# Performance work log

Hardware: AMD Instinct MI355X
Metric: run time of the kernel (lower is better)

The kernel has to match this reference:

```python
import jax, jax.numpy as jnp
import numpy as np

# Static config mirroring init_kwargs
N, C, H, W = 2, 10, 30, 30
PAD = 4                    # pad_size
HL = WL = 1 + 2 * PAD      # 9x9 local window
MAXH = MAXW = 10           # max_height / max_width
L = MAXH * MAXW            # tokens per pixel sequence = 100
D = C + 1                  # d_model = 11 (color channels + pad indicator)
EPS = 1e-5


def setup_inputs() -> dict:
    key = jax.random.key(0)
    ks = jax.random.split(key, 7)
    # one-hot ARC-style grid: each pixel is one of C colors
    classes = jax.random.randint(ks[0], (N, H, W), 0, C)
    x = jax.nn.one_hot(classes, C, dtype=jnp.float32).transpose(0, 3, 1, 2)  # [N,C,H,W]
    s = 0.1
    w_in = jax.random.normal(ks[1], (3 * D, D), dtype=jnp.float32) * s   # in_proj_weight
    w_out = jax.random.normal(ks[2], (D, D), dtype=jnp.float32) * s     # out_proj
    w_ff1 = jax.random.normal(ks[3], (1, D), dtype=jnp.float32) * s     # linear1 (D->1)
    w_ff2 = jax.random.normal(ks[4], (D, 1), dtype=jnp.float32) * s     # linear2 (1->D)
    ln1_g = jnp.ones((D,), dtype=jnp.float32)
    ln2_g = jnp.ones((D,), dtype=jnp.float32)
    return {"x": x, "w_in": w_in, "w_out": w_out, "w_ff1": w_ff1,
            "w_ff2": w_ff2, "ln1_g": ln1_g, "ln2_g": ln2_g}


def _layernorm(x, g):
    m = jnp.mean(x, axis=-1, keepdims=True)
    v = jnp.var(x, axis=-1, keepdims=True)
    return (x - m) / jnp.sqrt(v + EPS) * g


def reference(x, w_in, w_out, w_ff1, w_ff2, ln1_g, ln2_g):
    # pad colors with pad_value=0, pad-indicator channel with 1 in the border
    xp = jnp.pad(x, ((0, 0), (0, 0), (PAD, PAD), (PAD, PAD)))
    ind = jnp.pad(jnp.zeros((N, 1, H, W), x.dtype),
                  ((0, 0), (0, 0), (PAD, PAD), (PAD, PAD)), constant_values=1.0)
    xa = jnp.concatenate([xp, ind], axis=1).transpose(0, 2, 3, 1)  # [N,Hp,Wp,D]

    # im2col: 9x9 window around every pixel
    ii = jnp.arange(H)[:, None] + jnp.arange(HL)[None, :]  # [H,HL]
    jj = jnp.arange(W)[:, None] + jnp.arange(WL)[None, :]  # [W,WL]
    patches = xa[:, ii[:, None, :, None], jj[None, :, None, :], :]   # [N,H,W,HL,WL,D]
    patches = patches.transpose(0, 1, 2, 5, 3, 4)                    # [N,H,W,D,HL,WL]
    # embed window into max_height x max_width canvas (fill = pad_value = 0)
    patches = jnp.pad(patches, ((0, 0),) * 4 + ((0, MAXH - HL), (0, MAXW - WL)))
    seq = patches.reshape(N * H * W, D, L).transpose(0, 2, 1)        # [B,L,D]

    mask_inf = jnp.all(seq == 0, axis=2)               # [B,L] key padding mask
    mask0 = (seq[:, :, -1:] == 1).astype(seq.dtype)    # [B,L,1] border-padding gate

    # --- TransformerEncoderLayer (post-norm, bias=False, eval/no-dropout) ---
    qkv = seq @ w_in.T                                 # [B,L,3D]
    q, k, v = jnp.split(qkv, 3, axis=-1)
    # nhead = D, head_dim = 1, scale = 1/sqrt(1) = 1 -> per-channel outer products
    scores = jnp.einsum('bqd,bkd->bdqk', q, k)         # [B,D,L,L]
    scores = jnp.where(mask_inf[:, None, None, :], -1e9, scores)
    attn = jax.nn.softmax(scores, axis=-1)
    ao = jnp.einsum('bdqk,bkd->bqd', attn, v) @ w_out.T
    h = _layernorm(seq + ao, ln1_g)
    ff = jax.nn.relu(h @ w_ff1.T) @ w_ff2.T            # D -> 1 -> D
    h = _layernorm(h + ff, ln2_g)

    # softmax over color channels, zero out everywhere except padded border tokens
    colored = jax.nn.softmax(h[:, :, :-1], axis=2) * mask0
    out = (seq[:, :, :-1] + colored).transpose(0, 2, 1)  # [B,C,L]
    return out
```

## Files before the change

kernel.cpp:

```cpp
#include <hip/hip_runtime.h>

#define NB   2
#define CC   10
#define HH   30
#define WW   30
#define PADR 4
#define DD   11
#define NPIX (NB*HH*WW)
#define GP   16
#define PPB  4
#define NBLK (NPIX/PPB)

__global__ __launch_bounds__(256) void classify(const float* __restrict__ x,
                                                unsigned char* __restrict__ cm) {
    const int p = blockIdx.x * 256 + threadIdx.x;
    if (p >= NPIX) return;
    const int n  = p / (HH * WW);
    const int rm = p % (HH * WW);
    const float* xp = x + n * CC * HH * WW + rm;
    int c = 10;
    #pragma unroll
    for (int k = 0; k < CC; k++) {
        if (xp[k * HH * WW] > 0.5f) { c = k; break; }
    }
    cm[p] = (unsigned char)c;
}

__global__ __launch_bounds__(64) void emit(
    const float* __restrict__ w_in,
    const float* __restrict__ w_out,
    const float* __restrict__ w_ff1,
    const float* __restrict__ w_ff2,
    const float* __restrict__ ln1g,
    const float* __restrict__ ln2g,
    const unsigned char* __restrict__ cm,
    float* __restrict__ out)
{
    __shared__ float E[121];
    __shared__ float EV[121];
    __shared__ float WO[121];
    __shared__ float G1[11], G2[11], F1[11], F2[11];
    __shared__ unsigned char chs[PPB][100];

    const int t = threadIdx.x;

    for (int i = t; i < 121; i += 64) {
        const int d = i / 11, c = i % 11;
        const float Q = w_in[d * DD + 10];
        const float K = w_in[(DD + d) * DD + c];
        const float V = w_in[(2 * DD + d) * DD + c];
        const float e = __expf(Q * K);
        E[i] = e; EV[i] = e * V; WO[i] = w_out[i];
    }
    if (t < 11) { G1[t] = ln1g[t]; G2[t] = ln2g[t]; F1[t] = w_ff1[t]; F2[t] = w_ff2[t]; }

    const int grp = t >> 4;
    const int g   = t & 15;
    const int pix = blockIdx.x * PPB + grp;
    const int n  = pix / (HH * WW);
    const int rm = pix % (HH * WW);
    const int i0 = rm / WW, j0 = rm % WW;

    unsigned int pk0 = 0, pk1 = 0, pk2 = 0;
    for (int l = g; l < 100; l += GP) {
        const int ph = l / 10, pw = l % 10;
        unsigned int c = 255;
        if (ph < 9 && pw < 9) {
            const int r  = i0 + ph - PADR;
            const int cc = j0 + pw - PADR;
            c = 10;
            if (r >= 0 && r < HH && cc >= 0 && cc < WW)
                c = cm[n * HH * WW + r * WW + cc];
            const unsigned int inc = 1u << ((c & 3) * 8);
            if (c < 4) pk0 += inc; else if (c < 8) pk1 += inc; else pk2 += inc;
        }
        chs[grp][l] = (unsigned char)c;
    }
    __syncthreads();

    #pragma unroll
    for (int m = 1; m < GP; m <<= 1) {
        pk0 += __shfl_xor(pk0, m, GP);
        pk1 += __shfl_xor(pk1, m, GP);
        pk2 += __shfl_xor(pk2, m, GP);
    }
    float cnt[11];
    #pragma unroll
    for (int c = 0; c < 11; c++) {
        const unsigned int pk = (c < 4) ? pk0 : ((c < 8) ? pk1 : pk2);
        cnt[c] = (float)((pk >> ((c & 3) * 8)) & 0xFFu);
    }

    const int d = (g < 11) ? g : 0;

    float s1 = 0.f, s2 = 0.f;
    #pragma unroll
    for (int c = 0; c < 11; c++) {
        s1 += cnt[c] * E[d * 11 + c];
        s2 += cnt[c] * EV[d * 11 + c];
    }
    const float ao = s2 / s1;

    float h = 0.f;
    #pragma unroll
    for (int j = 0; j < 11; j++)
        h += WO[d * 11 + j] * __shfl(ao, j, GP);
    if (g == 10) h += 1.0f;
    if (g >= 11) h = 0.f;

    float s = h;
    #pragma unroll
    for (int m = 1; m < GP; m <<= 1) s += __shfl_xor(s, m, GP);
    float mean = s * (1.f / 11.f);
    float dv = (g < 11) ? (h - mean) : 0.f;
    float sq = dv * dv;
    #pragma unroll
    for (int m = 1; m < GP; m <<= 1) sq += __shfl_xor(sq, m, GP);
    const float hb = dv * rsqrtf(sq * (1.f / 11.f) + 1e-5f) * G1[d];

    float f = hb * F1[d];
    #pragma unroll
    for (int m = 1; m < GP; m <<= 1) f += __shfl_xor(f, m, GP);
    f = fmaxf(f, 0.f);
    float h2 = hb + f * F2[d];
    if (g >= 11) h2 = 0.f;

    s = h2;
    #pragma unroll
    for (int m = 1; m < GP; m <<= 1) s += __shfl_xor(s, m, GP);
    mean = s * (1.f / 11.f);
    dv = (g < 11) ? (h2 - mean) : 0.f;
    sq = dv * dv;
    #pragma unroll
    for (int m = 1; m < GP; m <<= 1) sq += __shfl_xor(sq, m, GP);
    const float hc = dv * rsqrtf(sq * (1.f / 11.f) + 1e-5f) * G2[d];

    float mv = (g < 10) ? hc : -1e30f;
    #pragma unroll
    for (int m = 1; m < GP; m <<= 1) mv = fmaxf(mv, __shfl_xor(mv, m, GP));
    const float ex = (g < 10) ? __expf(hc - mv) : 0.f;
    float den = ex;
    #pragma unroll
    for (int m = 1; m < GP; m <<= 1) den += __shfl_xor(den, m, GP);
    const float smv = ex / den;

    float* po = out + (size_t)pix * 1000;
    const unsigned char* chp = chs[grp];
    for (int vi = g; vi < 250; vi += GP) {
        const int idx = vi * 4;
        const int c   = idx / 100;
        const int l0  = idx - c * 100;
        const uchar4 c4 = *reinterpret_cast<const uchar4*>(chp + l0);
        const float sv = __shfl(smv, c, GP);
        float4 v4;
        v4.x = (c4.x == 255) ? 0.f : ((c4.x < 10) ? ((c == c4.x) ? 1.f : 0.f) : sv);
        v4.y = (c4.y == 255) ? 0.f : ((c4.y < 10) ? ((c == c4.y) ? 1.f : 0.f) : sv);
        v4.z = (c4.z == 255) ? 0.f : ((c4.z < 10) ? ((c == c4.z) ? 1.f : 0.f) : sv);
        v4.w = (c4.w == 255) ? 0.f : ((c4.w < 10) ? ((c == c4.w) ? 1.f : 0.f) : sv);
        reinterpret_cast<float4*>(po)[vi] = v4;
    }
}

extern "C" void kernel_launch(void* const* d_in, const int* in_sizes, int n_in,
                              void* d_out, int out_size, void* d_ws, size_t ws_size,
                              hipStream_t stream) {
    const float* x     = (const float*)d_in[0];
    const float* w_in  = (const float*)d_in[1];
    const float* w_out = (const float*)d_in[2];
    const float* w_ff1 = (const float*)d_in[3];
    const float* w_ff2 = (const float*)d_in[4];
    const float* ln1g  = (const float*)d_in[5];
    const float* ln2g  = (const float*)d_in[6];
    unsigned char* cm  = (unsigned char*)d_ws;
    float* out = (float*)d_out;

    classify<<<(NPIX + 255) / 256, 256, 0, stream>>>(x, cm);
    emit<<<NBLK, 64, 0, stream>>>(w_in, w_out, w_ff1, w_ff2, ln1g, ln2g, cm, out);
}
```

Before: 80.18 us.

## Use one 128-thread block per pixel with shared-memory atomic color counts

The emit kernel moves from four pixels per 64-thread block, where 16-lane groups handled each pixel, to one pixel per 128-thread block. Window color counts are now built with shared-memory atomics instead of packed-byte shuffle reductions. The per-channel math runs on 16 threads, and the softmax results pass through shared memory so all 128 threads can write the 1000-float output with float4 stores. This trades more blocks, and two extra syncs and a weight reload per pixel, for more threads writing each pixel's output.

Measured after the change: 76.86 us. 4.1% less time.

```diff
diff --git a/kernel.cpp b/kernel.cpp
--- a/kernel.cpp
+++ b/kernel.cpp
@@ -7,9 +7,6 @@
 #define PADR 4
 #define DD   11
 #define NPIX (NB*HH*WW)
-#define GP   16
-#define PPB  4
-#define NBLK (NPIX/PPB)
 
 __global__ __launch_bounds__(256) void classify(const float* __restrict__ x,
                                                 unsigned char* __restrict__ cm) {
@@ -26,7 +23,7 @@
     cm[p] = (unsigned char)c;
 }
 
-__global__ __launch_bounds__(64) void emit(
+__global__ __launch_bounds__(128) void emit(
     const float* __restrict__ w_in,
     const float* __restrict__ w_out,
     const float* __restrict__ w_ff1,
@@ -40,30 +37,33 @@
     __shared__ float EV[121];
     __shared__ float WO[121];
     __shared__ float G1[11], G2[11], F1[11], F2[11];
-    __shared__ unsigned char chs[PPB][100];
+    __shared__ int   cnt[11];
+    __shared__ float smvS[10];
+    __shared__ unsigned char chs[100];
 
     const int t = threadIdx.x;
+    const int pix = blockIdx.x;
+    const int n  = pix / (HH * WW);
+    const int rm = pix % (HH * WW);
+    const int i0 = rm / WW, j0 = rm % WW;
 
-    for (int i = t; i < 121; i += 64) {
-        const int d = i / 11, c = i % 11;
+    if (t < 121) {
+        const int d = t / 11, c = t % 11;
         const float Q = w_in[d * DD + 10];
         const float K = w_in[(DD + d) * DD + c];
         const float V = w_in[(2 * DD + d) * DD + c];
         const float e = __expf(Q * K);
-        E[i] = e; EV[i] = e * V; WO[i] = w_out[i];
+        E[t] = e; EV[t] = e * V; WO[t] = w_out[t];
     }
-    if (t < 11) { G1[t] = ln1g[t]; G2[t] = ln2g[t]; F1[t] = w_ff1[t]; F2[t] = w_ff2[t]; }
+    if (t < 11) {
+        G1[t] = ln1g[t]; G2[t] = ln2g[t];
+        F1[t] = w_ff1[t]; F2[t] = w_ff2[t];
+        cnt[t] = 0;
+    }
+    __syncthreads();
 
-    const int grp = t >> 4;
-    const int g   = t & 15;
-    const int pix = blockIdx.x * PPB + grp;
-    const int n  = pix / (HH * WW);
-    const int rm = pix % (HH * WW);
-    const int i0 = rm / WW, j0 = rm % WW;
-
-    unsigned int pk0 = 0, pk1 = 0, pk2 = 0;
-    for (int l = g; l < 100; l += GP) {
-        const int ph = l / 10, pw = l % 10;
+    if (t < 100) {
+        const int ph = t / 10, pw = t % 10;
         unsigned int c = 255;
         if (ph < 9 && pw < 9) {
             const int r  = i0 + ph - PADR;
@@ -71,93 +71,87 @@
             c = 10;
             if (r >= 0 && r < HH && cc >= 0 && cc < WW)
                 c = cm[n * HH * WW + r * WW + cc];
-            const unsigned int inc = 1u << ((c & 3) * 8);
-            if (c < 4) pk0 += inc; else if (c < 8) pk1 += inc; else pk2 += inc;
+            atomicAdd(&cnt[c], 1);
         }
-        chs[grp][l] = (unsigned char)c;
+        chs[t] = (unsigned char)c;
     }
     __syncthreads();
 
-    #pragma unroll
-    for (int m = 1; m < GP; m <<= 1) {
-        pk0 += __shfl_xor(pk0, m, GP);
-        pk1 += __shfl_xor(pk1, m, GP);
-        pk2 += __shfl_xor(pk2, m, GP);
+    if (t < 16) {
+        const int g = t;
+        const int d = (g < 11) ? g : 0;
+
+        float s1 = 0.f, s2 = 0.f;
+        #pragma unroll
+        for (int c = 0; c < 11; c++) {
+            const float cn = (float)cnt[c];
+            s1 += cn * E[d * 11 + c];
+            s2 += cn * EV[d * 11 + c];
+        }
+        const float ao = s2 / s1;
+
+        float h = 0.f;
+        #pragma unroll
+        for (int j = 0; j < 11; j++)
+            h += WO[d * 11 + j] * __shfl(ao, j, 16);
+        if (g == 10) h += 1.0f;
+        if (g >= 11) h = 0.f;
+
+        float s = h;
+        #pragma unroll
+        for (int m = 1; m < 16; m <<= 1) s += __shfl_xor(s, m, 16);
+        float mean = s * (1.f / 11.f);
+        float dv = (g < 11) ? (h - mean) : 0.f;
+        float sq = dv * dv;
+        #pragma unroll
+        for (int m = 1; m < 16; m <<= 1) sq += __shfl_xor(sq, m, 16);
+        const float hb = dv * rsqrtf(sq * (1.f / 11.f) + 1e-5f) * G1[d];
+
+        float f = hb * F1[d];
+        #pragma unroll
+        for (int m = 1; m < 16; m <<= 1) f += __shfl_xor(f, m, 16);
+        f = fmaxf(f, 0.f);
+        float h2 = hb + f * F2[d];
+        if (g >= 11) h2 = 0.f;
+
+        s = h2;
+        #pragma unroll
+        for (int m = 1; m < 16; m <<= 1) s += __shfl_xor(s, m, 16);
+        mean = s * (1.f / 11.f);
+        dv = (g < 11) ? (h2 - mean) : 0.f;
+        sq = dv * dv;
+        #pragma unroll
+        for (int m = 1; m < 16; m <<= 1) sq += __shfl_xor(sq, m, 16);
+        const float hc = dv * rsqrtf(sq * (1.f / 11.f) + 1e-5f) * G2[d];
+
+        float mv = (g < 10) ? hc : -1e30f;
+        #pragma unroll
+        for (int m = 1; m < 16; m <<= 1) mv = fmaxf(mv, __shfl_xor(mv, m, 16));
+        const float ex = (g < 10) ? __expf(hc - mv) : 0.f;
+        float den = ex;
+        #pragma unroll
+        for (int m = 1; m < 16; m <<= 1) den += __shfl_xor(den, m, 16);
+        if (g < 10) smvS[g] = ex / den;
     }
-    float cnt[11];
-    #pragma unroll
-    for (int c = 0; c < 11; c++) {
-        const unsigned int pk = (c < 4) ? pk0 : ((c < 8) ? pk1 : pk2);
-        cnt[c] = (float)((pk >> ((c & 3) * 8)) & 0xFFu);
-    }
-
-    const int d = (g < 11) ? g : 0;
-
-    float s1 = 0.f, s2 = 0.f;
-    #pragma unroll
-    for (int c = 0; c < 11; c++) {
-        s1 += cnt[c] * E[d * 11 + c];
-        s2 += cnt[c] * EV[d * 11 + c];
-    }
-    const float ao = s2 / s1;
-
-    float h = 0.f;
-    #pragma unroll
-    for (int j = 0; j < 11; j++)
-        h += WO[d * 11 + j] * __shfl(ao, j, GP);
-    if (g == 10) h += 1.0f;
-    if (g >= 11) h = 0.f;
-
-    float s = h;
-    #pragma unroll
-    for (int m = 1; m < GP; m <<= 1) s += __shfl_xor(s, m, GP);
-    float mean = s * (1.f / 11.f);
-    float dv = (g < 11) ? (h - mean) : 0.f;
-    float sq = dv * dv;
-    #pragma unroll
-    for (int m = 1; m < GP; m <<= 1) sq += __shfl_xor(sq, m, GP);
-    const float hb = dv * rsqrtf(sq * (1.f / 11.f) + 1e-5f) * G1[d];
-
-    float f = hb * F1[d];
-    #pragma unroll
-    for (int m = 1; m < GP; m <<= 1) f += __shfl_xor(f, m, GP);
-    f = fmaxf(f, 0.f);
-    float h2 = hb + f * F2[d];
-    if (g >= 11) h2 = 0.f;
-
-    s = h2;
-    #pragma unroll
-    for (int m = 1; m < GP; m <<= 1) s += __shfl_xor(s, m, GP);
-    mean = s * (1.f / 11.f);
-    dv = (g < 11) ? (h2 - mean) : 0.f;
-    sq = dv * dv;
-    #pragma unroll
-    for (int m = 1; m < GP; m <<= 1) sq += __shfl_xor(sq, m, GP);
-    const float hc = dv * rsqrtf(sq * (1.f / 11.f) + 1e-5f) * G2[d];
-
-    float mv = (g < 10) ? hc : -1e30f;
-    #pragma unroll
-    for (int m = 1; m < GP; m <<= 1) mv = fmaxf(mv, __shfl_xor(mv, m, GP));
-    const float ex = (g < 10) ? __expf(hc - mv) : 0.f;
-    float den = ex;
-    #pragma unroll
-    for (int m = 1; m < GP; m <<= 1) den += __shfl_xor(den, m, GP);
-    const float smv = ex / den;
+    __syncthreads();
 
     float* po = out + (size_t)pix * 1000;
-    const unsigned char* chp = chs[grp];
-    for (int vi = g; vi < 250; vi += GP) {
-        const int idx = vi * 4;
-        const int c   = idx / 100;
-        const int l0  = idx - c * 100;
-        const uchar4 c4 = *reinterpret_cast<const uchar4*>(chp + l0);
-        const float sv = __shfl(smv, c, GP);
-        float4 v4;
-        v4.x = (c4.x == 255) ? 0.f : ((c4.x < 10) ? ((c == c4.x) ? 1.f : 0.f) : sv);
-        v4.y = (c4.y == 255) ? 0.f : ((c4.y < 10) ? ((c == c4.y) ? 1.f : 0.f) : sv);
-        v4.z = (c4.z == 255) ? 0.f : ((c4.z < 10) ? ((c == c4.z) ? 1.f : 0.f) : sv);
-        v4.w = (c4.w == 255) ? 0.f : ((c4.w < 10) ? ((c == c4.w) ? 1.f : 0.f) : sv);
-        reinterpret_cast<float4*>(po)[vi] = v4;
+    #pragma unroll
+    for (int it = 0; it < 2; it++) {
+        const int vi = t + it * 128;
+        if (vi < 250) {
+            const int idx = vi * 4;
+            const int c   = idx / 100;
+            const int l0  = idx - c * 100;
+            const uchar4 c4 = *reinterpret_cast<const uchar4*>(chs + l0);
+            const float sv = smvS[c];
+            float4 v4;
+            v4.x = (c4.x == 255) ? 0.f : ((c4.x < 10) ? ((c == c4.x) ? 1.f : 0.f) : sv);
+            v4.y = (c4.y == 255) ? 0.f : ((c4.y < 10) ? ((c == c4.y) ? 1.f : 0.f) : sv);
+            v4.z = (c4.z == 255) ? 0.f : ((c4.z < 10) ? ((c == c4.z) ? 1.f : 0.f) : sv);
+            v4.w = (c4.w == 255) ? 0.f : ((c4.w < 10) ? ((c == c4.w) ? 1.f : 0.f) : sv);
+            reinterpret_cast<float4*>(po)[vi] = v4;
+        }
     }
 }
 
@@ -175,5 +169,5 @@
     float* out = (float*)d_out;
 
     classify<<<(NPIX + 255) / 256, 256, 0, stream>>>(x, cm);
-    emit<<<NBLK, 64, 0, stream>>>(w_in, w_out, w_ff1, w_ff2, ln1g, ln2g, cm, out);
+    emit<<<NPIX, 128, 0, stream>>>(w_in, w_out, w_ff1, w_ff2, ln1g, ln2g, cm, out);
 }
```
